# Optimization experiments

Measured on AMD Instinct MI355X. Metric: run time of the kernel, lower is better.

Reference implementation:

```python
import jax, jax.numpy as jnp
import numpy as np

B, T, D = 16, 512, 256
HS, D_A, R = 512, 64, 8


def setup_inputs() -> dict:
    key = jax.random.key(0)
    ks = jax.random.split(key, 8)
    s = lambda *sh: 1.0 / np.sqrt(sh[0])
    x = jax.random.normal(ks[0], (B, T, D), dtype=jnp.float32)
    w_first = jax.random.normal(ks[1], (D, D_A), dtype=jnp.float32) * s(D)
    b_first = jnp.zeros((D_A,), dtype=jnp.float32)
    w_second = jax.random.normal(ks[2], (D_A, R), dtype=jnp.float32) * s(D_A)
    b_second = jnp.zeros((R,), dtype=jnp.float32)
    weight_iBarh = jax.random.normal(ks[3], (D, 4 * HS), dtype=jnp.float32) * s(D)
    weight_hh = jax.random.normal(ks[4], (HS, 4 * HS), dtype=jnp.float32) * s(HS)
    bias = jnp.zeros((4 * HS,), dtype=jnp.float32)
    return {"x": x, "w_first": w_first, "b_first": b_first,
            "w_second": w_second, "b_second": b_second,
            "weight_iBarh": weight_iBarh, "weight_hh": weight_hh, "bias": bias}


def _forward(x, w_first, b_first, w_second, b_second, weight_iBarh, weight_hh, bias):
    b, t, d = x.shape
    hs = weight_hh.shape[0]
    r = w_second.shape[1]
    # attention logits for every timestep: (B, T, r)
    s = jnp.tanh(x @ w_first + b_first) @ w_second + b_second
    # causal mask: query t attends to keys j <= t
    mask = jnp.tril(jnp.ones((t, t), dtype=bool))  # (t_query, j_key)
    # logits: (B, Tq, Tk, r); softmax over key axis per (t, r), masked to prefix
    logits = jnp.where(mask[None, :, :, None], s[:, None, :, :], -jnp.inf)
    attn = jax.nn.softmax(logits, axis=2).mean(axis=-1)  # (B, Tq, Tk) == mean over r
    # M_t = attention-weighted average of prefix inputs: (B, T, D)
    M = jnp.einsum('btj,bjd->btd', attn, x)
    gates_x = jnp.einsum('btd,dg->btg', M, weight_iBarh) + bias  # (B, T, 4H)

    def step(carry, gx):
        h, c = carry
        g = gx + h @ weight_hh  # (B, 4H)
        i = jax.nn.sigmoid(g[:, :hs])
        f = jax.nn.sigmoid(g[:, hs:2 * hs])
        gg = jnp.tanh(g[:, 2 * hs:3 * hs])
        o = jax.nn.sigmoid(g[:, 3 * hs:])
        c = f * c + i * gg
        h = o * jnp.tanh(c)
        return (h, c), h

    h0 = jnp.zeros((b, hs), dtype=x.dtype)
    c0 = jnp.zeros((b, hs), dtype=x.dtype)
    (h_t, c_t), hseq = jax.lax.scan(step, (h0, c0), jnp.swapaxes(gates_x, 0, 1))
    hidden_seq = jnp.swapaxes(hseq, 0, 1)  # (B, T, H)
    return hidden_seq, h_t, c_t


def reference(x, w_first, b_first, w_second, b_second, weight_iBarh, weight_hh, bias):
    return _forward(x, w_first, b_first, w_second, b_second, weight_iBarh, weight_hh, bias)
```

## Files before the change

### kernel.cpp

```cpp
#include <hip/hip_runtime.h>
#include <math.h>

#define BB 16
#define TT 512
#define DD 256
#define HS 512
#define DA 64
#define RR 8
#define G4H 2048


__global__ __launch_bounds__(256) void k1_score(
    const float* __restrict__ x, const float* __restrict__ w1,
    const float* __restrict__ b1, const float* __restrict__ w2,
    const float* __restrict__ b2, float* __restrict__ s_out) {
  const int wave = threadIdx.x >> 6;
  const int lane = threadIdx.x & 63;
  for (int i = 0; i < 4; ++i) {
    const int bt = blockIdx.x * 16 + wave * 4 + i;
    const float* xr = x + bt * DD;
    float acc = b1[lane];
    #pragma unroll 4
    for (int d = 0; d < DD; ++d)
      acc = fmaf(xr[d], w1[d * DA + lane], acc);
    const float a = tanhf(acc);
    #pragma unroll
    for (int r = 0; r < RR; ++r) {
      float v = a * w2[lane * RR + r];
      for (int off = 32; off > 0; off >>= 1) v += __shfl_xor(v, off);
      if (lane == 0) s_out[bt * RR + r] = v + b2[r];
    }
  }
}

__global__ __launch_bounds__(512) void k2_prefix(
    const float* __restrict__ s_in, float* __restrict__ e_out,
    float* __restrict__ inv_out) {
  const int b = blockIdx.x >> 3, r = blockIdx.x & 7;
  const int t = threadIdx.x;
  __shared__ float red[TT];
  __shared__ float buf[2][TT];
  const float v = s_in[(b * TT + t) * RR + r];
  red[t] = v;
  __syncthreads();
  for (int off = 256; off >= 1; off >>= 1) {
    if (t < off) red[t] = fmaxf(red[t], red[t + off]);
    __syncthreads();
  }
  const float m = red[0];
  const float e = expf(v - m);
  int p = 0;
  buf[0][t] = e;
  __syncthreads();
  for (int off = 1; off < TT; off <<= 1) {
    const float add = (t >= off) ? buf[p][t - off] : 0.f;
    buf[1 - p][t] = buf[p][t] + add;
    __syncthreads();
    p ^= 1;
  }
  const float den = buf[p][t];
  e_out[(b * TT + t) * RR + r] = e;
  inv_out[(b * TT + t) * RR + r] = 1.0f / den;
}

__global__ __launch_bounds__(64) void k3_mix(
    const float* __restrict__ x, const float* __restrict__ e_in,
    const float* __restrict__ inv_in, float* __restrict__ Mout) {
  const int b = blockIdx.x >> 2;
  const int d = (blockIdx.x & 3) * 64 + threadIdx.x;
  __shared__ __align__(16) float el[TT * RR];
  __shared__ __align__(16) float il[TT * RR];
  for (int i = threadIdx.x * 4; i < TT * RR; i += 64 * 4) {
    *(float4*)&el[i] = *(const float4*)&e_in[b * TT * RR + i];
    *(float4*)&il[i] = *(const float4*)&inv_in[b * TT * RR + i];
  }
  __syncthreads();
  float4 c0 = {0.f, 0.f, 0.f, 0.f}, c1 = {0.f, 0.f, 0.f, 0.f};
  for (int t = 0; t < TT; ++t) {
    const float xv = x[(b * TT + t) * DD + d];
    const float4 e0 = *(const float4*)&el[t * RR];
    const float4 e1 = *(const float4*)&el[t * RR + 4];
    const float4 i0 = *(const float4*)&il[t * RR];
    const float4 i1 = *(const float4*)&il[t * RR + 4];
    c0.x = fmaf(e0.x, xv, c0.x); c0.y = fmaf(e0.y, xv, c0.y);
    c0.z = fmaf(e0.z, xv, c0.z); c0.w = fmaf(e0.w, xv, c0.w);
    c1.x = fmaf(e1.x, xv, c1.x); c1.y = fmaf(e1.y, xv, c1.y);
    c1.z = fmaf(e1.z, xv, c1.z); c1.w = fmaf(e1.w, xv, c1.w);
    float msum = c0.x * i0.x + c0.y * i0.y + c0.z * i0.z + c0.w * i0.w;
    msum += c1.x * i1.x + c1.y * i1.y + c1.z * i1.z + c1.w * i1.w;
    Mout[(b * TT + t) * DD + d] = msum * 0.125f;
  }
}

#define FMA4(ACC, W4, HSC)                         \
  ACC.x = fmaf((W4).x, (HSC), ACC.x);              \
  ACC.y = fmaf((W4).y, (HSC), ACC.y);              \
  ACC.z = fmaf((W4).z, (HSC), ACC.z);              \
  ACC.w = fmaf((W4).w, (HSC), ACC.w);

__device__ __forceinline__ float fast_sigmoid(float x) {
  return __builtin_amdgcn_rcpf(1.f + __expf(-x));
}
__device__ __forceinline__ float fast_tanh(float x) {
  const float xc = fmaxf(x, -30.f);
  const float e = __expf(-2.f * xc);
  return (1.f - e) * __builtin_amdgcn_rcpf(1.f + e);
}

#define HPOLL(Q) __hip_atomic_load((Q), __ATOMIC_RELAXED, __HIP_MEMORY_SCOPE_AGENT)

__global__ __launch_bounds__(512, 1) void k5_lstm(
    const float* __restrict__ Mrow, const float* __restrict__ whh,
    const float* __restrict__ wih, const float* __restrict__ bias,
    float* __restrict__ out, unsigned long long* hbuf) {
  const int s   = blockIdx.x & 15;
  const int b   = blockIdx.x >> 4;
  const int tid = threadIdx.x;
  const int kq  = tid & 15;
  const int cq  = tid >> 4;
  const int j0  = s * 32;
  const int unit = j0 + cq;

  __shared__ __align__(16) float Wl[32768];
  __shared__ __align__(16) float hl[2][576];
  __shared__ __align__(16) float M_lds[2][320];

  float4 wr[32];
  for (int rnd = 0; rnd < 2; ++rnd) {
    for (int i = tid * 4; i < 256 * 128; i += 512 * 4) {
      const int k = i >> 7, c = i & 127;
      *(float4*)&Wl[i] =
          *(const float4*)&whh[(rnd * 256 + k) * G4H + (c >> 5) * HS + j0 + (c & 31)];
    }
    __syncthreads();
    if ((kq >> 3) == rnd) {
      const int kb = (kq & 7) * 32;
      #pragma unroll
      for (int kk = 0; kk < 32; ++kk) {
        const int base = (kb + kk) * 128 + cq;
        wr[kk].x = *(volatile const float*)&Wl[base];
        wr[kk].y = *(volatile const float*)&Wl[base + 32];
        wr[kk].z = *(volatile const float*)&Wl[base + 64];
        wr[kk].w = *(volatile const float*)&Wl[base + 96];
      }
    }
    __syncthreads();
  }

  for (int m = tid * 4; m < 32768; m += 512 * 4) {
    const int wv = m >> 12;
    const int ii = (m >> 8) & 15;
    const int l  = (m >> 2) & 63;
    const int g_kq = l & 15, g_cq = wv * 4 + (l >> 4);
    const int row = g_kq * 16 + ii;
    float4 w4;
    w4.x = wih[row * G4H + 0 * HS + j0 + g_cq];
    w4.y = wih[row * G4H + 1 * HS + j0 + g_cq];
    w4.z = wih[row * G4H + 2 * HS + j0 + g_cq];
    w4.w = wih[row * G4H + 3 * HS + j0 + g_cq];
    *(float4*)&Wl[m] = w4;
  }
  if (tid < 64)
    *(float4*)&M_lds[0][(tid >> 2) * 20 + (tid & 3) * 4] =
        *(const float4*)&Mrow[(long)b * TT * DD + tid * 4];
  float bi = 0.f, bf = 0.f, bg = 0.f, bo = 0.f;
  if (kq == 0) {
    bi = bias[unit];          bf = bias[HS + unit];
    bg = bias[2 * HS + unit]; bo = bias[3 * HS + unit];
  }
  __syncthreads();

  float c_reg = 0.f;

  for (int t = 0; t < TT; ++t) {
    const int par = t & 1;
    float4 mnext = {0.f, 0.f, 0.f, 0.f};
    if (tid < 64) {
      const int tn = (t + 1 < TT) ? t + 1 : t;
      mnext = *(const float4*)&Mrow[((long)b * TT + tn) * DD + tid * 4];
    }
    float4 acc = {0.f, 0.f, 0.f, 0.f};
    {
      const float* Lp = &Wl[(cq >> 2) * 4096 + ((cq & 3) * 16 + kq) * 4];
      const float* mp = &M_lds[par][kq * 20];
      #pragma unroll
      for (int i = 0; i < 16; ++i) {
        const float4 w4 = *(const float4*)(Lp + i * 256);
        const float mv = mp[i];
        FMA4(acc, w4, mv);
      }
    }
    asm volatile("" : "+v"(acc.x), "+v"(acc.y), "+v"(acc.z), "+v"(acc.w));
    if (t > 0) {
      const unsigned long long* hsrc =
          hbuf + (((t - 1) & 1) * BB + b) * HS + tid;
      unsigned long long pkt;
      do { pkt = HPOLL(hsrc); } while ((unsigned)(pkt >> 32) < (unsigned)t);
      hl[par][(tid >> 5) * 36 + (tid & 31)] = __uint_as_float((unsigned)pkt);
    }
    if (tid < 64)
      *(float4*)&M_lds[par ^ 1][(tid >> 2) * 20 + (tid & 3) * 4] = mnext;
    __syncthreads();
    if (t > 0) {
      const float* hb = &hl[par][kq * 36];
      #pragma unroll
      for (int i = 0; i < 8; ++i) {
        const float4 h4 = *(const float4*)(hb + i * 4);
        FMA4(acc, wr[i * 4 + 0], h4.x);
        FMA4(acc, wr[i * 4 + 1], h4.y);
        FMA4(acc, wr[i * 4 + 2], h4.z);
        FMA4(acc, wr[i * 4 + 3], h4.w);
      }
    }
    #pragma unroll
    for (int off = 1; off <= 8; off <<= 1) {
      acc.x += __shfl_xor(acc.x, off); acc.y += __shfl_xor(acc.y, off);
      acc.z += __shfl_xor(acc.z, off); acc.w += __shfl_xor(acc.w, off);
    }
    if (kq == 0) {
      const float I = fast_sigmoid(acc.x + bi);
      const float F = fast_sigmoid(acc.y + bf);
      const float G = fast_tanh(acc.z + bg);
      const float O = fast_sigmoid(acc.w + bo);
      c_reg = F * c_reg + I * G;
      const float h = O * fast_tanh(c_reg);
      const unsigned long long pkt2 =
          ((unsigned long long)(unsigned)(t + 1) << 32) |
          (unsigned long long)__float_as_uint(h);
      __hip_atomic_store(&hbuf[((t & 1) * BB + b) * HS + unit], pkt2,
                         __ATOMIC_RELAXED, __HIP_MEMORY_SCOPE_AGENT);
      out[((long)b * TT + t) * HS + unit] = h;
      if (t == TT - 1) {
        out[(long)BB * TT * HS + b * HS + unit] = h;
        out[(long)BB * TT * HS + BB * HS + b * HS + unit] = c_reg;
      }
    }
  }
}

extern "C" void kernel_launch(void* const* d_in, const int* in_sizes, int n_in,
                              void* d_out, int out_size, void* d_ws,
                              size_t ws_size, hipStream_t stream) {
  const float* x    = (const float*)d_in[0];
  const float* w1   = (const float*)d_in[1];
  const float* b1   = (const float*)d_in[2];
  const float* w2   = (const float*)d_in[3];
  const float* b2   = (const float*)d_in[4];
  const float* wih  = (const float*)d_in[5];
  const float* whh  = (const float*)d_in[6];
  const float* bias = (const float*)d_in[7];
  float* out = (float*)d_out;

  float* ws = (float*)d_ws;
  float* s_buf  = ws;
  float* e_buf  = ws + 65536;
  float* i_buf  = ws + 131072;
  float* M_buf  = ws + 196608;
  unsigned long long* hbuf64 = (unsigned long long*)ws;

  k1_score<<<512, 256, 0, stream>>>(x, w1, b1, w2, b2, s_buf);
  k2_prefix<<<BB * RR, 512, 0, stream>>>(s_buf, e_buf, i_buf);
  k3_mix<<<64, 64, 0, stream>>>(x, e_buf, i_buf, M_buf);
  hipMemsetAsync(hbuf64, 0, 2 * BB * HS * sizeof(unsigned long long), stream);
  k5_lstm<<<256, 512, 0, stream>>>(M_buf, whh, wih, bias, out, hbuf64);
}
```

Before: 1.085 ms.

## Split prefix mixing into chunked partial sums plus scan, unroll LSTM polling

The serial prefix-weighted mixing kernel, which ran only 64 small blocks looping over all 512 timesteps, is replaced by two kernels. The first computes per-chunk partial sums over 64-step chunks, and the second adds up the earlier chunk partials and scans within its own chunk, giving 128 blocks of 256 threads. The LSTM hidden-state poll now keeps four outstanding atomic loads in flight to cut the latency of spinning on a single load. The score kernel also switches tanhf to a fast exp-based tanh. This adds a workspace buffer and a kernel launch, and slightly changes floating-point summation order.

```diff
diff --git a/kernel.cpp b/kernel.cpp
--- a/kernel.cpp
+++ b/kernel.cpp
@@ -9,6 +9,15 @@
 #define RR 8
 #define G4H 2048
 
+
+__device__ __forceinline__ float fast_sigmoid(float x) {
+  return __builtin_amdgcn_rcpf(1.f + __expf(-x));
+}
+__device__ __forceinline__ float fast_tanh(float x) {
+  const float xc = fmaxf(x, -30.f);
+  const float e = __expf(-2.f * xc);
+  return (1.f - e) * __builtin_amdgcn_rcpf(1.f + e);
+}
 
 __global__ __launch_bounds__(256) void k1_score(
     const float* __restrict__ x, const float* __restrict__ w1,
@@ -23,7 +32,7 @@
     #pragma unroll 4
     for (int d = 0; d < DD; ++d)
       acc = fmaf(xr[d], w1[d * DA + lane], acc);
-    const float a = tanhf(acc);
+    const float a = fast_tanh(acc);
     #pragma unroll
     for (int r = 0; r < RR; ++r) {
       float v = a * w2[lane * RR + r];
@@ -63,32 +72,71 @@
   inv_out[(b * TT + t) * RR + r] = 1.0f / den;
 }
 
-__global__ __launch_bounds__(64) void k3_mix(
+__global__ __launch_bounds__(256) void k3a_partial(
     const float* __restrict__ x, const float* __restrict__ e_in,
-    const float* __restrict__ inv_in, float* __restrict__ Mout) {
-  const int b = blockIdx.x >> 2;
-  const int d = (blockIdx.x & 3) * 64 + threadIdx.x;
-  __shared__ __align__(16) float el[TT * RR];
-  __shared__ __align__(16) float il[TT * RR];
-  for (int i = threadIdx.x * 4; i < TT * RR; i += 64 * 4) {
-    *(float4*)&el[i] = *(const float4*)&e_in[b * TT * RR + i];
-    *(float4*)&il[i] = *(const float4*)&inv_in[b * TT * RR + i];
-  }
-  __syncthreads();
-  float4 c0 = {0.f, 0.f, 0.f, 0.f}, c1 = {0.f, 0.f, 0.f, 0.f};
-  for (int t = 0; t < TT; ++t) {
+    float* __restrict__ Pbuf) {
+  const int b = blockIdx.x >> 3, ch = blockIdx.x & 7;
+  const int d = threadIdx.x;
+  __shared__ __align__(16) float el[64 * RR];
+  if (threadIdx.x < 128)
+    *(float4*)&el[threadIdx.x * 4] =
+        *(const float4*)&e_in[(b * TT + ch * 64) * RR + threadIdx.x * 4];
+  __syncthreads();
+  float p0 = 0.f, p1 = 0.f, p2 = 0.f, p3 = 0.f;
+  float p4 = 0.f, p5 = 0.f, p6 = 0.f, p7 = 0.f;
+  for (int j = 0; j < 64; ++j) {
+    const float xv = x[(b * TT + ch * 64 + j) * DD + d];
+    const float4 e0 = *(const float4*)&el[j * RR];
+    const float4 e1 = *(const float4*)&el[j * RR + 4];
+    p0 = fmaf(e0.x, xv, p0); p1 = fmaf(e0.y, xv, p1);
+    p2 = fmaf(e0.z, xv, p2); p3 = fmaf(e0.w, xv, p3);
+    p4 = fmaf(e1.x, xv, p4); p5 = fmaf(e1.y, xv, p5);
+    p6 = fmaf(e1.z, xv, p6); p7 = fmaf(e1.w, xv, p7);
+  }
+  float* pp = &Pbuf[((b * 8 + ch) * DD + d) * 8];
+  float4 o0 = {p0, p1, p2, p3}, o1 = {p4, p5, p6, p7};
+  *(float4*)pp = o0;
+  *(float4*)(pp + 4) = o1;
+}
+
+__global__ __launch_bounds__(256) void k3b_scan(
+    const float* __restrict__ x, const float* __restrict__ e_in,
+    const float* __restrict__ inv_in, const float* __restrict__ Pbuf,
+    float* __restrict__ Mout) {
+  const int b = blockIdx.x >> 3, ch = blockIdx.x & 7;
+  const int d = threadIdx.x;
+  __shared__ __align__(16) float el[64 * RR];
+  __shared__ __align__(16) float il[64 * RR];
+  if (threadIdx.x < 128) {
+    *(float4*)&el[threadIdx.x * 4] =
+        *(const float4*)&e_in[(b * TT + ch * 64) * RR + threadIdx.x * 4];
+    *(float4*)&il[threadIdx.x * 4] =
+        *(const float4*)&inv_in[(b * TT + ch * 64) * RR + threadIdx.x * 4];
+  }
+  __syncthreads();
+  float c0 = 0.f, c1 = 0.f, c2 = 0.f, c3 = 0.f;
+  float c4 = 0.f, c5 = 0.f, c6 = 0.f, c7 = 0.f;
+  for (int cp = 0; cp < ch; ++cp) {
+    const float* pp = &Pbuf[((b * 8 + cp) * DD + d) * 8];
+    const float4 a = *(const float4*)pp;
+    const float4 bb = *(const float4*)(pp + 4);
+    c0 += a.x; c1 += a.y; c2 += a.z; c3 += a.w;
+    c4 += bb.x; c5 += bb.y; c6 += bb.z; c7 += bb.w;
+  }
+  for (int j = 0; j < 64; ++j) {
+    const int t = ch * 64 + j;
     const float xv = x[(b * TT + t) * DD + d];
-    const float4 e0 = *(const float4*)&el[t * RR];
-    const float4 e1 = *(const float4*)&el[t * RR + 4];
-    const float4 i0 = *(const float4*)&il[t * RR];
-    const float4 i1 = *(const float4*)&il[t * RR + 4];
-    c0.x = fmaf(e0.x, xv, c0.x); c0.y = fmaf(e0.y, xv, c0.y);
-    c0.z = fmaf(e0.z, xv, c0.z); c0.w = fmaf(e0.w, xv, c0.w);
-    c1.x = fmaf(e1.x, xv, c1.x); c1.y = fmaf(e1.y, xv, c1.y);
-    c1.z = fmaf(e1.z, xv, c1.z); c1.w = fmaf(e1.w, xv, c1.w);
-    float msum = c0.x * i0.x + c0.y * i0.y + c0.z * i0.z + c0.w * i0.w;
-    msum += c1.x * i1.x + c1.y * i1.y + c1.z * i1.z + c1.w * i1.w;
-    Mout[(b * TT + t) * DD + d] = msum * 0.125f;
+    const float4 e0 = *(const float4*)&el[j * RR];
+    const float4 e1 = *(const float4*)&el[j * RR + 4];
+    const float4 i0 = *(const float4*)&il[j * RR];
+    const float4 i1 = *(const float4*)&il[j * RR + 4];
+    c0 = fmaf(e0.x, xv, c0); c1 = fmaf(e0.y, xv, c1);
+    c2 = fmaf(e0.z, xv, c2); c3 = fmaf(e0.w, xv, c3);
+    c4 = fmaf(e1.x, xv, c4); c5 = fmaf(e1.y, xv, c5);
+    c6 = fmaf(e1.z, xv, c6); c7 = fmaf(e1.w, xv, c7);
+    float m = c0 * i0.x + c1 * i0.y + c2 * i0.z + c3 * i0.w;
+    m += c4 * i1.x + c5 * i1.y + c6 * i1.z + c7 * i1.w;
+    Mout[(b * TT + t) * DD + d] = m * 0.125f;
   }
 }
 
@@ -97,15 +145,6 @@
   ACC.y = fmaf((W4).y, (HSC), ACC.y);              \
   ACC.z = fmaf((W4).z, (HSC), ACC.z);              \
   ACC.w = fmaf((W4).w, (HSC), ACC.w);
-
-__device__ __forceinline__ float fast_sigmoid(float x) {
-  return __builtin_amdgcn_rcpf(1.f + __expf(-x));
-}
-__device__ __forceinline__ float fast_tanh(float x) {
-  const float xc = fmaxf(x, -30.f);
-  const float e = __expf(-2.f * xc);
-  return (1.f - e) * __builtin_amdgcn_rcpf(1.f + e);
-}
 
 #define HPOLL(Q) __hip_atomic_load((Q), __ATOMIC_RELAXED, __HIP_MEMORY_SCOPE_AGENT)
 
@@ -194,8 +233,19 @@
     if (t > 0) {
       const unsigned long long* hsrc =
           hbuf + (((t - 1) & 1) * BB + b) * HS + tid;
-      unsigned long long pkt;
-      do { pkt = HPOLL(hsrc); } while ((unsigned)(pkt >> 32) < (unsigned)t);
+      const unsigned tt = (unsigned)t;
+      unsigned long long q0, q1, q2, q3, pkt;
+      q0 = HPOLL(hsrc); q1 = HPOLL(hsrc); q2 = HPOLL(hsrc); q3 = HPOLL(hsrc);
+      for (;;) {
+        if ((unsigned)(q0 >> 32) >= tt) { pkt = q0; break; }
+        q0 = HPOLL(hsrc);
+        if ((unsigned)(q1 >> 32) >= tt) { pkt = q1; break; }
+        q1 = HPOLL(hsrc);
+        if ((unsigned)(q2 >> 32) >= tt) { pkt = q2; break; }
+        q2 = HPOLL(hsrc);
+        if ((unsigned)(q3 >> 32) >= tt) { pkt = q3; break; }
+        q3 = HPOLL(hsrc);
+      }
       hl[par][(tid >> 5) * 36 + (tid & 31)] = __uint_as_float((unsigned)pkt);
     }
     if (tid < 64)
@@ -256,11 +306,13 @@
   float* e_buf  = ws + 65536;
   float* i_buf  = ws + 131072;
   float* M_buf  = ws + 196608;
+  float* P_buf  = ws + 2293760;
   unsigned long long* hbuf64 = (unsigned long long*)ws;
 
   k1_score<<<512, 256, 0, stream>>>(x, w1, b1, w2, b2, s_buf);
   k2_prefix<<<BB * RR, 512, 0, stream>>>(s_buf, e_buf, i_buf);
-  k3_mix<<<64, 64, 0, stream>>>(x, e_buf, i_buf, M_buf);
+  k3a_partial<<<BB * 8, 256, 0, stream>>>(x, e_buf, P_buf);
+  k3b_scan<<<BB * 8, 256, 0, stream>>>(x, e_buf, i_buf, P_buf, M_buf);
   hipMemsetAsync(hbuf64, 0, 2 * BB * HS * sizeof(unsigned long long), stream);
   k5_lstm<<<256, 512, 0, stream>>>(M_buf, whh, wih, bias, out, hbuf64);
 }
```

After: 1.160 ms. 6.9% more time.
